# Performance work log

Measured on AMD Instinct MI355X. Metric: run time of the kernel, lower is better.

## Reference

```python
import math
import jax
import jax.numpy as jnp
import numpy as np
from jax import lax

N_FEATURES = 51
WINDOW = 100
EMBED = 12
HIDDEN = math.ceil(0.6 * WINDOW)  # 60
N_PRUNE = math.ceil(0.6 * N_FEATURES * N_FEATURES)  # 1561
BATCH = 8192


def setup_inputs() -> dict:
    key = jax.random.key(0)
    ks = jax.random.split(key, 8)
    x = jax.random.normal(ks[0], (BATCH * N_FEATURES, WINDOW), dtype=jnp.float32)
    embed = jax.random.normal(ks[1], (N_FEATURES, EMBED), dtype=jnp.float32)
    fin = WINDOW + EMBED
    gcn_w = jax.random.normal(ks[2], (WINDOW, fin), dtype=jnp.float32) * (1.0 / np.sqrt(fin))
    gcn_b = jnp.zeros((WINDOW,), dtype=jnp.float32)
    w1 = jax.random.normal(ks[3], (HIDDEN, WINDOW), dtype=jnp.float32) * (1.0 / np.sqrt(WINDOW))
    b1 = jnp.zeros((HIDDEN,), dtype=jnp.float32)
    w2 = jax.random.normal(ks[4], (WINDOW, HIDDEN), dtype=jnp.float32) * (1.0 / np.sqrt(HIDDEN))
    b2 = jnp.zeros((WINDOW,), dtype=jnp.float32)
    return {"x": x, "batch_size": BATCH, "embed": embed, "gcn_w": gcn_w,
            "gcn_b": gcn_b, "w1": w1, "b1": b1, "w2": w2, "b2": b2}


def _prune(A, n):
    """Faithful translation of the serial greedy prune loop."""
    N = A.shape[0]

    def cond(st):
        _, i = st
        return i < n

    def body(st):
        A, i = st
        idx = jnp.argmin(A)
        r, c = idx // N, idx % N
        v = A[r, c]
        ok = ((jnp.sum(A[r]) - v) > 0) | ((jnp.sum(A[:, c]) - v) > 0)
        newval = jnp.where(ok, jnp.float32(0.0), jnp.max(A))
        return (A.at[r, c].set(newval), i + jnp.where(ok, 1, 0))

    A, _ = lax.while_loop(cond, body, (A, jnp.int32(0)))
    return A


def _forward(x, batch_size, embed, gcn_w, gcn_b, w1, b1, w2, b2):
    # --- graph construction from detached embeddings ---
    weights = lax.stop_gradient(embed)                      # [N, E]
    nrm = jnp.linalg.norm(weights, axis=-1)                 # [N]
    cos = (weights @ weights.T) / (nrm[:, None] * nrm[None, :])
    A = _prune(cos, N_PRUNE)
    A = (A != 0).astype(x.dtype)                            # binary adjacency [N, N]
    # GCNConv symmetric normalization with added self-loops
    A_hat = A + jnp.eye(N_FEATURES, dtype=x.dtype)
    dinv = 1.0 / jnp.sqrt(jnp.sum(A_hat, axis=1))
    norm_adj = dinv[:, None] * A_hat * dinv[None, :]        # [N, N]

    # --- features: concat window with node embeddings ---
    all_emb = jnp.tile(embed, (batch_size, 1))              # [B*N, E]
    h = jnp.concatenate([x, all_emb], axis=1)               # [B*N, W+E]
    h = h.reshape(batch_size, N_FEATURES, WINDOW + EMBED)   # [B, N, F]

    # GCNConv: linear transform then normalized aggregation (dropout in eval mode)
    h = h @ gcn_w.T                                         # [B, N, W]
    h = jnp.einsum('ij,bjw->biw', norm_adj, h) + gcn_b      # [B, N, W]
    h = jax.nn.relu(h).reshape(batch_size * N_FEATURES, WINDOW)

    # MLP: Linear -> tanh -> Linear -> tanh
    h = jnp.tanh(h @ w1.T + b1)
    h = jnp.tanh(h @ w2.T + b2)
    return h


def reference(x, batch_size, embed, gcn_w, gcn_b, w1, b1, w2, b2):
    return _forward(x, batch_size, embed, gcn_w, gcn_b, w1, b1, w2, b2)
```

## Files before the change

kernel.cpp:

```cpp
#include <hip/hip_runtime.h>
#include <hip/hip_bf16.h>
#include <stdint.h>

#define NF 51
#define NF2 (51*51)
#define WIN 100
#define EMB 12
#define FIN 112
#define HID 60
#define NPRUNE 1561
#define SORTN 4096

#define WS_WX    0
#define WS_W1    30464
#define WS_ADJ   47872
#define WS_W2    57088
#define WS_D     73216
#define WS_STAGE 47872
#define WS_TOTAL 96064

#define LDS_WX   0
#define LDS_W1   30464
#define LDS_R1X  47872
#define LDS_R1H  79152
#define LDS_R2   110432
#define LDS_TOTAL 142688

typedef _Float16 f16;
typedef _Float16 f16x8 __attribute__((ext_vector_type(8)));
typedef _Float16 f16x4 __attribute__((ext_vector_type(4)));
typedef float f32x4 __attribute__((ext_vector_type(4)));

__device__ __forceinline__ float fast_tanh(float x) {
  float xa = fminf(fmaxf(x, -15.f), 15.f);
  float e = __expf(2.f * xa);
  return (e - 1.f) * __builtin_amdgcn_rcpf(e + 1.f);
}

#define BAR() do { asm volatile("s_waitcnt lgkmcnt(0)" ::: "memory"); \
  __builtin_amdgcn_s_barrier(); asm volatile("" ::: "memory"); } while (0)

__global__ __launch_bounds__(512) void prune_kernel(const float* __restrict__ embed,
                                                    const float* __restrict__ gcn_w,
                                                    const float* __restrict__ gcn_b,
                                                    const float* __restrict__ w1,
                                                    const float* __restrict__ w2,
                                                    void* __restrict__ ws) {
  const int t = threadIdx.x;
  char* wsb = (char*)ws;

  if (blockIdx.x == 1) {
    f16* wxT = (f16*)(wsb + WS_WX);
    for (int u = t; u < 112*136; u += 512) {
      int nn = u / 136, k = u - nn*136;
      wxT[u] = (f16)((nn < WIN && k < WIN) ? gcn_w[nn*FIN + k] : 0.f);
    }
    f16* w1T = (f16*)(wsb + WS_W1);
    for (int u = t; u < 64*136; u += 512) {
      int nn = u / 136, k = u - nn*136;
      w1T[u] = (f16)((nn < HID && k < WIN) ? w1[nn*WIN + k] : 0.f);
    }
    f16* w2T = (f16*)(wsb + WS_W2);
    for (int u = t; u < 112*72; u += 512) {
      int nn = u / 72, k = u - nn*72;
      w2T[u] = (f16)((nn < WIN && k < HID) ? w2[nn*HID + k] : 0.f);
    }
    return;
  }

  __shared__ float sA[NF * 52];
  __shared__ unsigned long long sKey[SORTN];
  __shared__ float sNrm[NF];
  __shared__ float sDinv[NF];
  __shared__ float sRow[NF];
  __shared__ float sCol[NF];
  __shared__ float sRowS[NF];
  __shared__ float sColS[NF];
  __shared__ float sEmb[NF * EMB];
  __shared__ float sE2[NF * EMB];
  __shared__ unsigned char sMask[NF2];
  __shared__ unsigned long long sSusp[64];
  __shared__ int sCand[256];
  __shared__ int sCnt[17];
  __shared__ int sNS;
  __shared__ int sNC;
  __shared__ int sTotal;

  for (int u = t; u < NF * EMB; u += 512) sEmb[u] = embed[u];
  for (int u = t; u < NF2; u += 512) sMask[u] = 0;
  if (t == 0) { sNS = 0; sNC = 0; sTotal = 0; }
  __syncthreads();
  if (t < NF) {
    float s = 0.f;
    for (int e = 0; e < EMB; e++) { float w = sEmb[t*EMB + e]; s += w * w; }
    sNrm[t] = sqrtf(s);
  }
  __syncthreads();
  for (int u = t; u < NF2; u += 512) {
    int r = u / NF, c = u % NF;
    float d = 0.f;
    for (int e = 0; e < EMB; e++) d += sEmb[r*EMB + e] * sEmb[c*EMB + e];
    sA[r*52 + c] = d / (sNrm[r] * sNrm[c]);
  }
  __syncthreads();

  if (t < NF) {
    float rs = 0.f, cs = 0.f;
    for (int j = 0; j < NF; j++) { rs += sA[t*52 + j]; cs += sA[j*52 + t]; }
    sRow[t] = rs; sCol[t] = cs;
  }
  __syncthreads();

  {
    int myCnt = 0;
    for (int u = t; u < NF2; u += 512) {
      int r = u / NF, c = u % NF;
      float v = sA[r*52 + c];
      if (v < 0.f) {
        myCnt++;
        if (sRow[r] <= v && sCol[c] <= v) {
          int slot = atomicAdd(&sNC, 1);
          if (slot < 256) sCand[slot] = u;
        }
      }
    }
    if (myCnt) atomicAdd(&sTotal, myCnt);
  }
  __syncthreads();
  if (sNC <= 256) {
    const int nC = sNC;
    for (int i = t; i < nC; i += 512) {
      int u = sCand[i];
      int r = u / NF, c = u - r*NF;
      float v = sA[r*52 + c];
      float Pr = 0.f, Pc = 0.f;
      for (int j = 0; j < NF; j++) {
        float a = sA[r*52 + j];
        if (a < 0.f && (a < v || (a == v && r*NF + j < u))) Pr -= a;
        float b = sA[j*52 + c];
        if (b < 0.f && (b < v || (b == v && j*NF + c < u))) Pc -= b;
      }
      bool okS = ((sRow[r] + Pr - v) > 0.f) || ((sCol[c] + Pc - v) > 0.f);
      if (!okS) {
        int slot = atomicAdd(&sNS, 1);
        if (slot < 64) {
          unsigned int b = __float_as_uint(v);
          sSusp[slot] = ((unsigned long long)(~b) << 32) | (unsigned int)u;
          sMask[u] = 1;
        }
      }
    }
  }
  __syncthreads();
  const bool fastPath = (sTotal > 0) && (sTotal <= NPRUNE) && (sNC <= 256) && (sNS <= 64);

  if (fastPath) {
    if (t < 64) {
      const int lane = t;
      float mx = -3.0e38f;
      for (int u = lane; u < NF2; u += 64) mx = fmaxf(mx, sA[(u / NF)*52 + (u % NF)]);
      for (int o = 32; o > 0; o >>= 1) mx = fmaxf(mx, __shfl_xor(mx, o, 64));
      if (lane < NF) { sRowS[lane] = 0.f; sColS[lane] = 0.f; }
      const int nS = sNS;
      unsigned long long key = (lane < nS) ? sSusp[lane] : ~0ull;
      for (int k = 2; k <= 64; k <<= 1) {
        for (int j = k >> 1; j > 0; j >>= 1) {
          unsigned long long other = __shfl_xor(key, j, 64);
          bool up = ((lane & k) == 0);
          bool takeMin = (((lane & j) == 0) == up);
          unsigned long long mn = key < other ? key : other;
          unsigned long long mxk = key < other ? other : key;
          key = takeMin ? mn : mxk;
        }
      }
      for (int kk = 0; kk < nS; kk++) {
        unsigned long long kv = __shfl(key, kk, 64);
        unsigned int mb = (unsigned int)(kv >> 32);
        unsigned int idx = (unsigned int)kv;
        float v = __uint_as_float(~mb);
        int r = (int)(idx / NF), c = (int)(idx % NF);
        float pr = 0.f, pc = 0.f;
        if (lane < NF) {
          float a = sA[r*52 + lane];
          if (a < 0.f && !sMask[r*NF + lane] &&
              (a < v || (a == v && (unsigned)(r*NF + lane) < idx))) pr = -a;
          float b = sA[lane*52 + c];
          if (b < 0.f && !sMask[lane*NF + c] &&
              (b < v || (b == v && (unsigned)(lane*NF + c) < idx))) pc = -b;
        }
        for (int o = 32; o > 0; o >>= 1) {
          pr += __shfl_xor(pr, o, 64);
          pc += __shfl_xor(pc, o, 64);
        }
        float sumR = sRow[r] + pr + sRowS[r];
        float sumC = sCol[c] + pc + sColS[c];
        bool ok = ((sumR - v) > 0.f) || ((sumC - v) > 0.f);
        if (lane == 0) {
          if (ok) { sA[r*52 + c] = 0.f; sRowS[r] += -v;     sColS[c] += -v; }
          else    { sA[r*52 + c] = mx;  sRowS[r] += mx - v; sColS[c] += mx - v; }
        }
      }
    }
    __syncthreads();
    for (int u = t; u < NF2; u += 512) {
      int r = u / NF, c = u % NF;
      if (sA[r*52 + c] < 0.f) sA[r*52 + c] = 0.f;
    }
  } else {
    int myCnt = 0;
    for (int u = t; u < NF2; u += 512)
      myCnt += (sA[(u / NF)*52 + (u % NF)] < 0.f) ? 1 : 0;
    int incl = myCnt;
    for (int o = 1; o < 64; o <<= 1) {
      int nb = __shfl_up(incl, o, 64);
      if ((t & 63) >= o) incl += nb;
    }
    if ((t & 63) == 63) sCnt[t >> 6] = incl;
    __syncthreads();
    if (t == 0) {
      int run = 0;
      for (int j = 0; j < 8; j++) { int v = sCnt[j]; sCnt[8 + j] = run; run += v; }
      sCnt[16] = run;
    }
    __syncthreads();
    const int total = sCnt[16];
    const int n = (total <= 2048) ? 2048 : SORTN;
    {
      int cpos = sCnt[8 + (t >> 6)] + (incl - myCnt);
      for (int u = t; u < NF2; u += 512) {
        float v = sA[(u / NF)*52 + (u % NF)];
        if (v < 0.f) {
          unsigned int b = __float_as_uint(v);
          sKey[cpos++] = ((unsigned long long)(~b) << 32) | (unsigned int)u;
        }
      }
      for (int u = total + t; u < n; u += 512) sKey[u] = ~0ull;
    }
    __syncthreads();
    for (int kk = 2; kk <= n; kk <<= 1) {
      for (int jj = kk >> 1; jj > 0; jj >>= 1) {
        for (int u = t; u < n; u += 512) {
          int l = u ^ jj;
          if (l > u) {
            unsigned long long a = sKey[u], b = sKey[l];
            bool up = ((u & kk) == 0);
            if ((a > b) == up) { sKey[u] = b; sKey[l] = a; }
          }
        }
        __syncthreads();
      }
    }

    if (t < 64) {
      const int lane = t;
      float mx = -3.0e38f;
      for (int u = lane; u < NF2; u += 64) mx = fmaxf(mx, sA[(u / NF)*52 + (u % NF)]);
      for (int o = 32; o > 0; o >>= 1) mx = fmaxf(mx, __shfl_xor(mx, o, 64));

      int pruned = 0, pos = 0;
      bool toP2 = false;
      while (pruned < NPRUNE && !toP2) {
        int myi = pos + lane;
        unsigned long long kv = (myi < n) ? sKey[myi] : ~0ull;
        unsigned int mb  = (unsigned int)(kv >> 32);
        unsigned int idx = (unsigned int)kv;
        unsigned int vb  = (mb & 0x80000000u) ? (mb & 0x7FFFFFFFu) : ~mb;
        float v = __uint_as_float(vb);
        bool elig = (v < 0.f) && (idx < (unsigned)NF2);
        int r = 0, c2 = 0; bool okl = false;
        if (elig) {
          r = (int)(idx / NF); c2 = (int)(idx % NF);
          float sr = sRow[r], sc = sCol[c2];
          okl = ((sr - v) > 0.f) || ((sc - v) > 0.f);
        }
        unsigned long long bal = __ballot(okl);
        unsigned long long nb = ~bal;
        int nok = (nb == 0ull) ? 64 : (int)__builtin_ctzll(nb);
        int rem = NPRUNE - pruned;
        int take = nok < rem ? nok : rem;
        if (lane < take) {
          sA[r*52 + c2] = 0.f;
          atomicAdd(&sRow[r], -v);
          atomicAdd(&sCol[c2], -v);
        }
        pruned += take; pos += take;
        if (pruned >= NPRUNE) break;
        if (take == 64) continue;
        unsigned int bvb = (unsigned int)__builtin_amdgcn_readlane((int)vb, take);
        int bidx = __builtin_amdgcn_readlane((int)idx, take);
        float bv = __uint_as_float(bvb);
        if (!(bv < 0.f) || bidx >= NF2) { toP2 = true; break; }
        int br = bidx / NF, bc = bidx % NF;
        float sr = sRow[br], sc = sCol[bc];
        bool ok = ((sr - bv) > 0.f) || ((sc - bv) > 0.f);
        if (ok) {
          if (lane == 0) {
            sA[br*52 + bc] = 0.f;
            sRow[br] = sr - bv; sCol[bc] = sc - bv;
          }
          pruned++; pos++;
        } else {
          if (lane == 0) {
            sA[br*52 + bc] = mx;
            sRow[br] = sr + (mx - bv); sCol[bc] = sc + (mx - bv);
          }
          pos++;
        }
      }
      if (toP2) {
        for (int guard = 0; guard < 40000 && pruned < NPRUNE; guard++) {
          float bv = 3.0e38f; int bidx = NF2;
          for (int u = lane; u < NF2; u += 64) {
            float v = sA[(u / NF)*52 + (u % NF)];
            if (v < bv) { bv = v; bidx = u; }
          }
          for (int o = 32; o > 0; o >>= 1) {
            float ov = __shfl_xor(bv, o, 64);
            int  oi = __shfl_xor(bidx, o, 64);
            if (ov < bv || (ov == bv && oi < bidx)) { bv = ov; bidx = oi; }
          }
          int br = bidx / NF, bc = bidx % NF;
          float sr = sRow[br], sc = sCol[bc];
          bool ok = ((sr - bv) > 0.f) || ((sc - bv) > 0.f);
          if (ok) {
            if (bv == 0.f) break;
            if (lane == 0) { sA[br*52+bc] = 0.f; sRow[br] = sr - bv; sCol[bc] = sc - bv; }
            pruned++;
          } else {
            if (bv == mx) break;
            if (lane == 0) { sA[br*52+bc] = mx; sRow[br] = sr + (mx-bv); sCol[bc] = sc + (mx-bv); }
          }
        }
      }
    }
  }
  __syncthreads();

  if (t < NF) {
    float deg = 0.f;
    for (int j = 0; j < NF; j++) {
      float a = sA[t*52 + j];
      float bin = (a != 0.f) ? 1.f : 0.f;
      if (j == t) bin += 1.f;
      deg += bin;
    }
    sDinv[t] = 1.f / sqrtf(deg);
  }
  __syncthreads();

  float* sN = (float*)sKey;
  for (int u = t; u < NF * 52; u += 512) {
    int r = u / 52, c = u % 52;
    float v = 0.f;
    if (c < NF) {
      float a = sA[r*52 + c];
      float bin = (a != 0.f) ? 1.f : 0.f;
      if (r == c) bin += 1.f;
      v = sDinv[r] * bin * sDinv[c];
    }
    sN[u] = v;
  }
  __syncthreads();

  for (int u = t; u < NF * EMB; u += 512) {
    int i = u / EMB, e = u % EMB;
    float s2 = 0.f;
    for (int j = 0; j < NF; j++) s2 += sN[i*52 + j] * sEmb[j*EMB + e];
    sE2[u] = s2;
  }

  f16* adjT = (f16*)(wsb + WS_ADJ);
  for (int u = t; u < 64*72; u += 512) {
    int r = u / 72, k = u % 72;
    adjT[u] = (f16)((r < NF && k < NF) ? sN[r*52 + k] : 0.f);
  }
  __syncthreads();
  float* Dp = (float*)(wsb + WS_D);
  for (int u = t; u < NF * 112; u += 512) {
    int i = u / 112, w = u % 112;
    float s2 = 0.f;
    if (w < WIN) {
      for (int e = 0; e < EMB; e++) s2 += sE2[i*EMB + e] * gcn_w[w*FIN + WIN + e];
      s2 += gcn_b[w];
    }
    Dp[u] = s2;
  }
}

__global__ __launch_bounds__(512, 1) void forward_kernel(
    const float* __restrict__ x, const float* __restrict__ b1g,
    const float* __restrict__ b2g, const void* __restrict__ ws,
    float* __restrict__ out, int nPairs, int ppb) {
  __shared__ __align__(16) char smem[LDS_TOTAL];
  f16* wxT = (f16*)(smem + LDS_WX);
  f16* w1T = (f16*)(smem + LDS_W1);
  f16* sX  = (f16*)(smem + LDS_R1X);
  f16* sH  = (f16*)(smem + LDS_R1H);
  f16* yT  = (f16*)(smem + LDS_R2);
  f16* h3  = (f16*)(smem + LDS_R2);

  const int t = threadIdx.x;
  const int wv = t >> 6, lane = t & 63;
  const int c = lane & 15, g = lane >> 4;
  const int s = wv >> 2, mt = wv & 3;
  const int rowA = 51*s + 16*mt + c;

  {
    const f32x4* w4 = (const f32x4*)ws;
    f32x4* s4 = (f32x4*)smem;
    #pragma unroll
    for (int u = 0; u < 6; u++) { int i = t + u*512; if (i < 2992) s4[i] = w4[i]; }
    f32x4 z = {0.f,0.f,0.f,0.f};
    f32x4* za = (f32x4*)(smem + LDS_R1X);
    #pragma unroll
    for (int u = 0; u < 12; u++) { int i = t + u*512; if (i < 5926) za[i] = z; }
  }

  const int pair0 = blockIdx.x * ppb;
  float4 p0, p1, p2, p3, p4;
  if (pair0 < nPairs) {
    const float4* xb = (const float4*)(x + (size_t)pair0 * 10200);
    p0 = xb[t]; p1 = xb[t+512]; p2 = xb[t+1024]; p3 = xb[t+1536];
    if (t < 502) p4 = xb[t+2048];
  }

  const char* wsb = (const char*)ws;
  const f16* adjG = (const f16*)(wsb + WS_ADJ);
  const f16* w2G  = (const f16*)(wsb + WS_W2);
  const float* DG = (const float*)(wsb + WS_D);

  f16x8 adjf[4][2];
  #pragma unroll
  for (int N = 0; N < 4; N++) {
    const f16* bp = &adjG[(16*N + c)*72 + 8*g];
    adjf[N][0] = *(const f16x8*)(bp + 0);
    adjf[N][1] = *(const f16x8*)(bp + 32);
  }
  f16x8 w2f[7][2];
  #pragma unroll
  for (int N = 0; N < 7; N++) {
    const f16* ap = &w2G[(16*N + c)*72 + 8*g];
    w2f[N][0] = *(const f16x8*)(ap + 0);
    w2f[N][1] = *(const f16x8*)(ap + 32);
  }
  const int s2a = (wv == 7) ? 1 : 0;
  const int wta = (wv == 7) ? 0 : wv;
  const int wtb = wv + 1;
  float4 dA[4], dB[4];
  {
    const float4 zf = {0.f,0.f,0.f,0.f};
    #pragma unroll
    for (int N = 0; N < 4; N++) {
      int nd = 16*N + c;
      dA[N] = (nd < NF) ? *(const float4*)&DG[nd*112 + 16*wta + 4*g] : zf;
      dB[N] = (wv < 6 && nd < NF) ? *(const float4*)&DG[nd*112 + 16*wtb + 4*g] : zf;
    }
  }
  float4 b1f[4], b2f[7];
  {
    const float4 zf = {0.f,0.f,0.f,0.f};
    #pragma unroll
    for (int N = 0; N < 4; N++) {
      int colb = 16*N + 4*g;
      b1f[N] = (colb < HID) ? *(const float4*)&b1g[colb] : zf;
    }
    #pragma unroll
    for (int N = 0; N < 7; N++) {
      int colb = 16*N + 4*g;
      b2f[N] = (colb < WIN) ? *(const float4*)&b2g[colb] : zf;
    }
  }
  __syncthreads();

  if (pair0 < nPairs) {
    #define STV(PV, V) { int row = (V)/25, q4 = ((V)%25)*4; \
      f16x4 hv = {(f16)(PV).x,(f16)(PV).y,(f16)(PV).z,(f16)(PV).w}; \
      *(f16x4*)&sX[row*136 + q4] = hv; }
    STV(p0, t); STV(p1, t+512); STV(p2, t+1024); STV(p3, t+1536);
    if (t < 502) STV(p4, t+2048);
  }

  #pragma unroll 1
  for (int p = 0; p < ppb; p++) {
    const int pairIdx = pair0 + p;
    const bool valid = pairIdx < nPairs;

    BAR();

    if (p + 1 < ppb && pairIdx + 1 < nPairs) {
      const float4* xb = (const float4*)(x + (size_t)(pairIdx+1) * 10200);
      p0 = xb[t]; p1 = xb[t+512]; p2 = xb[t+1024]; p3 = xb[t+1536];
      if (t < 502) p4 = xb[t+2048];
    }

    if (valid) {
      const f16* aB = &sX[rowA*136];
      const f16x8 a0 = *(const f16x8*)(aB +  0 + 8*g);
      const f16x8 a1 = *(const f16x8*)(aB + 32 + 8*g);
      const f16x8 a2 = *(const f16x8*)(aB + 64 + 8*g);
      const f16x8 a3 = *(const f16x8*)(aB + 96 + 8*g);
      f16* yTs = yT + s*8064;
      const int nodeW = 16*mt + 4*g;
      #pragma unroll
      for (int N = 0; N < 7; N++) {
        const f16* bp = &wxT[(16*N + c)*136 + 8*g];
        f32x4 acc = {0.f,0.f,0.f,0.f};
        acc = __builtin_amdgcn_mfma_f32_16x16x32_f16(a0, *(const f16x8*)(bp +  0), acc, 0, 0, 0);
        acc = __builtin_amdgcn_mfma_f32_16x16x32_f16(a1, *(const f16x8*)(bp + 32), acc, 0, 0, 0);
        acc = __builtin_amdgcn_mfma_f32_16x16x32_f16(a2, *(const f16x8*)(bp + 64), acc, 0, 0, 0);
        acc = __builtin_amdgcn_mfma_f32_16x16x32_f16(a3, *(const f16x8*)(bp + 96), acc, 0, 0, 0);
        const int col = 16*N + c;
        if (mt < 3) {
          f16x4 hv = {(f16)acc[0],(f16)acc[1],(f16)acc[2],(f16)acc[3]};
          *(f16x4*)&yTs[col*72 + nodeW] = hv;
        } else {
          #pragma unroll
          for (int r2 = 0; r2 < 4; r2++)
            if (nodeW + r2 < NF) yTs[col*72 + nodeW + r2] = (f16)acc[r2];
        }
      }
    }
    BAR();

    if (valid) {
      {
        const f16* ap = &yT[s2a*8064 + (16*wta + c)*72 + 8*g];
        const f16x8 a0 = *(const f16x8*)(ap + 0);
        const f16x8 a1 = *(const f16x8*)(ap + 32);
        #pragma unroll
        for (int N = 0; N < 4; N++) {
          f32x4 acc = {0.f,0.f,0.f,0.f};
          acc = __builtin_amdgcn_mfma_f32_16x16x32_f16(a0, adjf[N][0], acc, 0, 0, 0);
          acc = __builtin_amdgcn_mfma_f32_16x16x32_f16(a1, adjf[N][1], acc, 0, 0, 0);
          const int nd = 16*N + c;
          if (nd < NF) {
            const float4 dv = dA[N];
            f16x4 hv = {(f16)fmaxf(acc[0]+dv.x,0.f),(f16)fmaxf(acc[1]+dv.y,0.f),
                        (f16)fmaxf(acc[2]+dv.z,0.f),(f16)fmaxf(acc[3]+dv.w,0.f)};
            *(f16x4*)&sH[(51*s2a + nd)*136 + 16*wta + 4*g] = hv;
          }
        }
      }
      if (wv < 6) {
        const f16* ap = &yT[8064 + (16*wtb + c)*72 + 8*g];
        const f16x8 a0 = *(const f16x8*)(ap + 0);
        const f16x8 a1 = *(const f16x8*)(ap + 32);
        #pragma unroll
        for (int N = 0; N < 4; N++) {
          f32x4 acc = {0.f,0.f,0.f,0.f};
          acc = __builtin_amdgcn_mfma_f32_16x16x32_f16(a0, adjf[N][0], acc, 0, 0, 0);
          acc = __builtin_amdgcn_mfma_f32_16x16x32_f16(a1, adjf[N][1], acc, 0, 0, 0);
          const int nd = 16*N + c;
          if (nd < NF) {
            const float4 dv = dB[N];
            f16x4 hv = {(f16)fmaxf(acc[0]+dv.x,0.f),(f16)fmaxf(acc[1]+dv.y,0.f),
                        (f16)fmaxf(acc[2]+dv.z,0.f),(f16)fmaxf(acc[3]+dv.w,0.f)};
            *(f16x4*)&sH[(51 + nd)*136 + 16*wtb + 4*g] = hv;
          }
        }
      }
    }
    BAR();

    if (valid) {
      const f16* bB = &sH[rowA*136 + 8*g];
      const f16x8 hb0 = *(const f16x8*)(bB +  0);
      const f16x8 hb1 = *(const f16x8*)(bB + 32);
      const f16x8 hb2 = *(const f16x8*)(bB + 64);
      const f16x8 hb3 = *(const f16x8*)(bB + 96);
      #pragma unroll
      for (int N = 0; N < 4; N++) {
        const f16* ap = &w1T[(16*N + c)*136 + 8*g];
        f32x4 acc = {0.f,0.f,0.f,0.f};
        acc = __builtin_amdgcn_mfma_f32_16x16x32_f16(*(const f16x8*)(ap +  0), hb0, acc, 0, 0, 0);
        acc = __builtin_amdgcn_mfma_f32_16x16x32_f16(*(const f16x8*)(ap + 32), hb1, acc, 0, 0, 0);
        acc = __builtin_amdgcn_mfma_f32_16x16x32_f16(*(const f16x8*)(ap + 64), hb2, acc, 0, 0, 0);
        acc = __builtin_amdgcn_mfma_f32_16x16x32_f16(*(const f16x8*)(ap + 96), hb3, acc, 0, 0, 0);
        const int colb = 16*N + 4*g;
        const float4 bv = b1f[N];
        f16x4 hv = {(f16)fast_tanh(acc[0]+bv.x),(f16)fast_tanh(acc[1]+bv.y),
                    (f16)fast_tanh(acc[2]+bv.z),(f16)fast_tanh(acc[3]+bv.w)};
        *(f16x4*)&h3[rowA*72 + colb] = hv;
      }
    }
    asm volatile("s_waitcnt lgkmcnt(0)" ::: "memory");
    __builtin_amdgcn_sched_barrier(0);

    if (valid) {
      const f16* bB = &h3[rowA*72 + 8*g];
      const f16x8 hb0 = *(const f16x8*)(bB +  0);
      const f16x8 hb1 = *(const f16x8*)(bB + 32);
      const bool rowOk = (16*mt + c) < NF;
      float* ob = out + (size_t)pairIdx * 10200 + (size_t)rowA * 100;
      #pragma unroll
      for (int N = 0; N < 7; N++) {
        f32x4 acc = {0.f,0.f,0.f,0.f};
        acc = __builtin_amdgcn_mfma_f32_16x16x32_f16(w2f[N][0], hb0, acc, 0, 0, 0);
        acc = __builtin_amdgcn_mfma_f32_16x16x32_f16(w2f[N][1], hb1, acc, 0, 0, 0);
        const int colb = 16*N + 4*g;
        if (rowOk && colb < WIN) {
          const float4 bv = b2f[N];
          float4 ov = {fast_tanh(acc[0]+bv.x), fast_tanh(acc[1]+bv.y),
                       fast_tanh(acc[2]+bv.z), fast_tanh(acc[3]+bv.w)};
          *(float4*)&ob[colb] = ov;
        }
      }
    }

    if (p + 1 < ppb && pairIdx + 1 < nPairs) {
      #define STV2(PV, V) { int row = (V)/25, q4 = ((V)%25)*4; \
        f16x4 hv = {(f16)(PV).x,(f16)(PV).y,(f16)(PV).z,(f16)(PV).w}; \
        *(f16x4*)&sX[row*136 + q4] = hv; }
      STV2(p0, t); STV2(p1, t+512); STV2(p2, t+1024); STV2(p3, t+1536);
      if (t < 502) STV2(p4, t+2048);
      #undef STV2
    }
  }
}

extern "C" void kernel_launch(void* const* d_in, const int* in_sizes, int n_in,
                              void* d_out, int out_size, void* d_ws, size_t ws_size,
                              hipStream_t stream) {
  const float* x     = (const float*)d_in[0];
  const float* embed = (const float*)d_in[2];
  const float* gcn_w = (const float*)d_in[3];
  const float* gcn_b = (const float*)d_in[4];
  const float* w1    = (const float*)d_in[5];
  const float* b1    = (const float*)d_in[6];
  const float* w2    = (const float*)d_in[7];
  const float* b2    = (const float*)d_in[8];
  float* out = (float*)d_out;

  const int batch = in_sizes[0] / (NF * WIN);
  const int nPairs = batch / 2;
  const int blocks = 256;
  const int ppb = (nPairs + blocks - 1) / blocks;

  prune_kernel<<<2, 512, 0, stream>>>(embed, gcn_w, gcn_b, w1, w2, d_ws);
  forward_kernel<<<blocks, 512, 0, stream>>>(x, b1, b2, d_ws, out, nPairs, ppb);
}
```

Before: 133.0 us.

## Split block into two 4-wave groups running staggered three-phase sample pipeline

The block now works as two independent 4-wave groups, each with its own LDS region and 16 samples. The three stages (GCN linear, adjacency aggregation, MLP plus store) run as phases, and the second group is offset by one phase. The intent is that different stages from the two groups overlap between barriers, so MFMA, LDS and global-store work interleave instead of all waves doing the same stage at once. In exchange, each sample needs three barrier-separated steps, LDS use grows slightly, and work per barrier interval is uneven between the groups.

```diff
diff --git a/kernel.cpp b/kernel.cpp
--- a/kernel.cpp
+++ b/kernel.cpp
@@ -10,6 +10,7 @@
 #define HID 60
 #define NPRUNE 1561
 #define SORTN 4096
+#define NPG 16
 
 #define WS_WX    0
 #define WS_W1    30464
@@ -21,10 +22,9 @@
 
 #define LDS_WX   0
 #define LDS_W1   30464
-#define LDS_R1X  47872
-#define LDS_R1H  79152
-#define LDS_R2   110432
-#define LDS_TOTAL 142688
+#define LDS_GRP  47872
+#define GRP_SPAN 50944
+#define LDS_TOTAL 149760
 
 typedef _Float16 f16;
 typedef _Float16 f16x8 __attribute__((ext_vector_type(8)));
@@ -390,20 +390,22 @@
 __global__ __launch_bounds__(512, 1) void forward_kernel(
     const float* __restrict__ x, const float* __restrict__ b1g,
     const float* __restrict__ b2g, const void* __restrict__ ws,
-    float* __restrict__ out, int nPairs, int ppb) {
+    float* __restrict__ out, int nSamp) {
   __shared__ __align__(16) char smem[LDS_TOTAL];
   f16* wxT = (f16*)(smem + LDS_WX);
   f16* w1T = (f16*)(smem + LDS_W1);
-  f16* sX  = (f16*)(smem + LDS_R1X);
-  f16* sH  = (f16*)(smem + LDS_R1H);
-  f16* yT  = (f16*)(smem + LDS_R2);
-  f16* h3  = (f16*)(smem + LDS_R2);
 
   const int t = threadIdx.x;
   const int wv = t >> 6, lane = t & 63;
+  const int gq = wv >> 2, wq = wv & 3;
+  const int tl = t & 255;
   const int c = lane & 15, g = lane >> 4;
-  const int s = wv >> 2, mt = wv & 3;
-  const int rowA = 51*s + 16*mt + c;
+  const int rowA1 = 16*wq + c;
+  char* grp = smem + LDS_GRP + gq * GRP_SPAN;
+  f16* sXg = (f16*)(grp);
+  f16* sHg = (f16*)(grp + 17408);
+  f16* yTg = (f16*)(grp + 34816);
+  f16* h3g = yTg;
 
   {
     const f32x4* w4 = (const f32x4*)ws;
@@ -411,17 +413,9 @@
     #pragma unroll
     for (int u = 0; u < 6; u++) { int i = t + u*512; if (i < 2992) s4[i] = w4[i]; }
     f32x4 z = {0.f,0.f,0.f,0.f};
-    f32x4* za = (f32x4*)(smem + LDS_R1X);
+    f32x4* za = (f32x4*)(smem + LDS_GRP);
     #pragma unroll
-    for (int u = 0; u < 12; u++) { int i = t + u*512; if (i < 5926) za[i] = z; }
-  }
-
-  const int pair0 = blockIdx.x * ppb;
-  float4 p0, p1, p2, p3, p4;
-  if (pair0 < nPairs) {
-    const float4* xb = (const float4*)(x + (size_t)pair0 * 10200);
-    p0 = xb[t]; p1 = xb[t+512]; p2 = xb[t+1024]; p3 = xb[t+1536];
-    if (t < 502) p4 = xb[t+2048];
+    for (int u = 0; u < 13; u++) { int i = t + u*512; if (i < 6368) za[i] = z; }
   }
 
   const char* wsb = (const char*)ws;
@@ -443,17 +437,14 @@
     w2f[N][0] = *(const f16x8*)(ap + 0);
     w2f[N][1] = *(const f16x8*)(ap + 32);
   }
-  const int s2a = (wv == 7) ? 1 : 0;
-  const int wta = (wv == 7) ? 0 : wv;
-  const int wtb = wv + 1;
   float4 dA[4], dB[4];
   {
     const float4 zf = {0.f,0.f,0.f,0.f};
     #pragma unroll
     for (int N = 0; N < 4; N++) {
       int nd = 16*N + c;
-      dA[N] = (nd < NF) ? *(const float4*)&DG[nd*112 + 16*wta + 4*g] : zf;
-      dB[N] = (wv < 6 && nd < NF) ? *(const float4*)&DG[nd*112 + 16*wtb + 4*g] : zf;
+      dA[N] = (nd < NF) ? *(const float4*)&DG[nd*112 + 16*wq + 4*g] : zf;
+      dB[N] = (wq < 3 && nd < NF) ? *(const float4*)&DG[nd*112 + 16*(wq+4) + 4*g] : zf;
     }
   }
   float4 b1f[4], b2f[7];
@@ -472,150 +463,151 @@
   }
   __syncthreads();
 
-  if (pair0 < nPairs) {
-    #define STV(PV, V) { int row = (V)/25, q4 = ((V)%25)*4; \
-      f16x4 hv = {(f16)(PV).x,(f16)(PV).y,(f16)(PV).z,(f16)(PV).w}; \
-      *(f16x4*)&sX[row*136 + q4] = hv; }
-    STV(p0, t); STV(p1, t+512); STV(p2, t+1024); STV(p3, t+1536);
-    if (t < 502) STV(p4, t+2048);
-  }
+  const int sBase = blockIdx.x * (2*NPG) + gq * NPG;
+  float4 p0, p1, p2, p3, p4;
+  #define LOADP(SI) { const float4* xb = (const float4*)(x + (size_t)(SI) * 5100); \
+    p0 = xb[tl]; p1 = xb[tl+256]; p2 = xb[tl+512]; p3 = xb[tl+768]; \
+    if (tl < 251) p4 = xb[tl+1024]; }
+  #define STV1(PV, V) { int row = (V)/25, q4 = ((V)%25)*4; \
+    f16x4 hv = {(f16)(PV).x,(f16)(PV).y,(f16)(PV).z,(f16)(PV).w}; \
+    *(f16x4*)&sXg[row*136 + q4] = hv; }
+  #define STVX() { STV1(p0, tl) STV1(p1, tl+256) STV1(p2, tl+512) STV1(p3, tl+768) \
+                   if (tl < 251) STV1(p4, tl+1024) }
+
+  if (sBase < nSamp) LOADP(sBase);
+  if (gq == 0) {
+    if (sBase < nSamp) STVX();
+    if (sBase + 1 < nSamp) LOADP(sBase + 1);
+  }
+  BAR();
+
+  const int phS1 = gq ? 1 : 0;
+  const int phS2 = gq ? 2 : 1;
 
   #pragma unroll 1
-  for (int p = 0; p < ppb; p++) {
-    const int pairIdx = pair0 + p;
-    const bool valid = pairIdx < nPairs;
-
-    BAR();
-
-    if (p + 1 < ppb && pairIdx + 1 < nPairs) {
-      const float4* xb = (const float4*)(x + (size_t)(pairIdx+1) * 10200);
-      p0 = xb[t]; p1 = xb[t+512]; p2 = xb[t+1024]; p3 = xb[t+1536];
-      if (t < 502) p4 = xb[t+2048];
-    }
-
-    if (valid) {
-      const f16* aB = &sX[rowA*136];
-      const f16x8 a0 = *(const f16x8*)(aB +  0 + 8*g);
-      const f16x8 a1 = *(const f16x8*)(aB + 32 + 8*g);
-      const f16x8 a2 = *(const f16x8*)(aB + 64 + 8*g);
-      const f16x8 a3 = *(const f16x8*)(aB + 96 + 8*g);
-      f16* yTs = yT + s*8064;
-      const int nodeW = 16*mt + 4*g;
-      #pragma unroll
-      for (int N = 0; N < 7; N++) {
-        const f16* bp = &wxT[(16*N + c)*136 + 8*g];
-        f32x4 acc = {0.f,0.f,0.f,0.f};
-        acc = __builtin_amdgcn_mfma_f32_16x16x32_f16(a0, *(const f16x8*)(bp +  0), acc, 0, 0, 0);
-        acc = __builtin_amdgcn_mfma_f32_16x16x32_f16(a1, *(const f16x8*)(bp + 32), acc, 0, 0, 0);
-        acc = __builtin_amdgcn_mfma_f32_16x16x32_f16(a2, *(const f16x8*)(bp + 64), acc, 0, 0, 0);
-        acc = __builtin_amdgcn_mfma_f32_16x16x32_f16(a3, *(const f16x8*)(bp + 96), acc, 0, 0, 0);
-        const int col = 16*N + c;
-        if (mt < 3) {
-          f16x4 hv = {(f16)acc[0],(f16)acc[1],(f16)acc[2],(f16)acc[3]};
-          *(f16x4*)&yTs[col*72 + nodeW] = hv;
-        } else {
+  for (int k = 0; k < 3*NPG + 1; k++) {
+    const int ph = k % 3;
+    const int kd3 = k / 3;
+    const f32x4 zacc = {0.f,0.f,0.f,0.f};
+
+    if (ph == phS1) {
+      if (kd3 < NPG && sBase + kd3 < nSamp) {
+        const f16* aB = &sXg[rowA1*136];
+        const f16x8 a0 = *(const f16x8*)(aB +  0 + 8*g);
+        const f16x8 a1 = *(const f16x8*)(aB + 32 + 8*g);
+        const f16x8 a2 = *(const f16x8*)(aB + 64 + 8*g);
+        const f16x8 a3 = *(const f16x8*)(aB + 96 + 8*g);
+        const int nodeW = 16*wq + 4*g;
+        #pragma unroll
+        for (int N = 0; N < 7; N++) {
+          const f16* bp = &wxT[(16*N + c)*136 + 8*g];
+          f32x4 acc = zacc;
+          acc = __builtin_amdgcn_mfma_f32_16x16x32_f16(a0, *(const f16x8*)(bp +  0), acc, 0, 0, 0);
+          acc = __builtin_amdgcn_mfma_f32_16x16x32_f16(a1, *(const f16x8*)(bp + 32), acc, 0, 0, 0);
+          acc = __builtin_amdgcn_mfma_f32_16x16x32_f16(a2, *(const f16x8*)(bp + 64), acc, 0, 0, 0);
+          acc = __builtin_amdgcn_mfma_f32_16x16x32_f16(a3, *(const f16x8*)(bp + 96), acc, 0, 0, 0);
+          const int col = 16*N + c;
+          if (wq < 3) {
+            f16x4 hv = {(f16)acc[0],(f16)acc[1],(f16)acc[2],(f16)acc[3]};
+            *(f16x4*)&yTg[col*72 + nodeW] = hv;
+          } else {
+            #pragma unroll
+            for (int r2 = 0; r2 < 4; r2++)
+              if (nodeW + r2 < NF) yTg[col*72 + nodeW + r2] = (f16)acc[r2];
+          }
+        }
+      }
+    } else if (ph == phS2) {
+      if (kd3 < NPG && sBase + kd3 < nSamp) {
+        {
+          const f16* ap = &yTg[(16*wq + c)*72 + 8*g];
+          const f16x8 a0 = *(const f16x8*)(ap + 0);
+          const f16x8 a1 = *(const f16x8*)(ap + 32);
           #pragma unroll
-          for (int r2 = 0; r2 < 4; r2++)
-            if (nodeW + r2 < NF) yTs[col*72 + nodeW + r2] = (f16)acc[r2];
-        }
-      }
-    }
-    BAR();
-
-    if (valid) {
-      {
-        const f16* ap = &yT[s2a*8064 + (16*wta + c)*72 + 8*g];
-        const f16x8 a0 = *(const f16x8*)(ap + 0);
-        const f16x8 a1 = *(const f16x8*)(ap + 32);
+          for (int N = 0; N < 4; N++) {
+            f32x4 acc = zacc;
+            acc = __builtin_amdgcn_mfma_f32_16x16x32_f16(a0, adjf[N][0], acc, 0, 0, 0);
+            acc = __builtin_amdgcn_mfma_f32_16x16x32_f16(a1, adjf[N][1], acc, 0, 0, 0);
+            const int nd = 16*N + c;
+            if (nd < NF) {
+              const float4 dv = dA[N];
+              f16x4 hv = {(f16)fmaxf(acc[0]+dv.x,0.f),(f16)fmaxf(acc[1]+dv.y,0.f),
+                          (f16)fmaxf(acc[2]+dv.z,0.f),(f16)fmaxf(acc[3]+dv.w,0.f)};
+              *(f16x4*)&sHg[nd*136 + 16*wq + 4*g] = hv;
+            }
+          }
+        }
+        if (wq < 3) {
+          const f16* ap = &yTg[(16*(wq+4) + c)*72 + 8*g];
+          const f16x8 a0 = *(const f16x8*)(ap + 0);
+          const f16x8 a1 = *(const f16x8*)(ap + 32);
+          #pragma unroll
+          for (int N = 0; N < 4; N++) {
+            f32x4 acc = zacc;
+            acc = __builtin_amdgcn_mfma_f32_16x16x32_f16(a0, adjf[N][0], acc, 0, 0, 0);
+            acc = __builtin_amdgcn_mfma_f32_16x16x32_f16(a1, adjf[N][1], acc, 0, 0, 0);
+            const int nd = 16*N + c;
+            if (nd < NF) {
+              const float4 dv = dB[N];
+              f16x4 hv = {(f16)fmaxf(acc[0]+dv.x,0.f),(f16)fmaxf(acc[1]+dv.y,0.f),
+                          (f16)fmaxf(acc[2]+dv.z,0.f),(f16)fmaxf(acc[3]+dv.w,0.f)};
+              *(f16x4*)&sHg[nd*136 + 16*(wq+4) + 4*g] = hv;
+            }
+          }
+        }
+      }
+    } else {
+      const int m = kd3 - gq;
+      if (m >= 0 && m < NPG && sBase + m < nSamp) {
+        const int sIdx = sBase + m;
+        const f16* bB = &sHg[rowA1*136 + 8*g];
+        const f16x8 hb0 = *(const f16x8*)(bB +  0);
+        const f16x8 hb1 = *(const f16x8*)(bB + 32);
+        const f16x8 hb2 = *(const f16x8*)(bB + 64);
+        const f16x8 hb3 = *(const f16x8*)(bB + 96);
         #pragma unroll
         for (int N = 0; N < 4; N++) {
-          f32x4 acc = {0.f,0.f,0.f,0.f};
-          acc = __builtin_amdgcn_mfma_f32_16x16x32_f16(a0, adjf[N][0], acc, 0, 0, 0);
-          acc = __builtin_amdgcn_mfma_f32_16x16x32_f16(a1, adjf[N][1], acc, 0, 0, 0);
-          const int nd = 16*N + c;
-          if (nd < NF) {
-            const float4 dv = dA[N];
-            f16x4 hv = {(f16)fmaxf(acc[0]+dv.x,0.f),(f16)fmaxf(acc[1]+dv.y,0.f),
-                        (f16)fmaxf(acc[2]+dv.z,0.f),(f16)fmaxf(acc[3]+dv.w,0.f)};
-            *(f16x4*)&sH[(51*s2a + nd)*136 + 16*wta + 4*g] = hv;
-          }
-        }
-      }
-      if (wv < 6) {
-        const f16* ap = &yT[8064 + (16*wtb + c)*72 + 8*g];
-        const f16x8 a0 = *(const f16x8*)(ap + 0);
-        const f16x8 a1 = *(const f16x8*)(ap + 32);
+          const f16* ap = &w1T[(16*N + c)*136 + 8*g];
+          f32x4 acc = zacc;
+          acc = __builtin_amdgcn_mfma_f32_16x16x32_f16(*(const f16x8*)(ap +  0), hb0, acc, 0, 0, 0);
+          acc = __builtin_amdgcn_mfma_f32_16x16x32_f16(*(const f16x8*)(ap + 32), hb1, acc, 0, 0, 0);
+          acc = __builtin_amdgcn_mfma_f32_16x16x32_f16(*(const f16x8*)(ap + 64), hb2, acc, 0, 0, 0);
+          acc = __builtin_amdgcn_mfma_f32_16x16x32_f16(*(const f16x8*)(ap + 96), hb3, acc, 0, 0, 0);
+          const int colb = 16*N + 4*g;
+          const float4 bv = b1f[N];
+          f16x4 hv = {(f16)fast_tanh(acc[0]+bv.x),(f16)fast_tanh(acc[1]+bv.y),
+                      (f16)fast_tanh(acc[2]+bv.z),(f16)fast_tanh(acc[3]+bv.w)};
+          *(f16x4*)&h3g[rowA1*72 + colb] = hv;
+        }
+        asm volatile("s_waitcnt lgkmcnt(0)" ::: "memory");
+        __builtin_amdgcn_sched_barrier(0);
+        const f16* bC = &h3g[rowA1*72 + 8*g];
+        const f16x8 hc0 = *(const f16x8*)(bC +  0);
+        const f16x8 hc1 = *(const f16x8*)(bC + 32);
+        const bool rowOk = rowA1 < NF;
+        float* ob = out + (size_t)sIdx * 5100 + (size_t)rowA1 * 100;
         #pragma unroll
-        for (int N = 0; N < 4; N++) {
-          f32x4 acc = {0.f,0.f,0.f,0.f};
-          acc = __builtin_amdgcn_mfma_f32_16x16x32_f16(a0, adjf[N][0], acc, 0, 0, 0);
-          acc = __builtin_amdgcn_mfma_f32_16x16x32_f16(a1, adjf[N][1], acc, 0, 0, 0);
-          const int nd = 16*N + c;
-          if (nd < NF) {
-            const float4 dv = dB[N];
-            f16x4 hv = {(f16)fmaxf(acc[0]+dv.x,0.f),(f16)fmaxf(acc[1]+dv.y,0.f),
-                        (f16)fmaxf(acc[2]+dv.z,0.f),(f16)fmaxf(acc[3]+dv.w,0.f)};
-            *(f16x4*)&sH[(51 + nd)*136 + 16*wtb + 4*g] = hv;
-          }
-        }
-      }
+        for (int N = 0; N < 7; N++) {
+          f32x4 acc = zacc;
+          acc = __builtin_amdgcn_mfma_f32_16x16x32_f16(w2f[N][0], hc0, acc, 0, 0, 0);
+          acc = __builtin_amdgcn_mfma_f32_16x16x32_f16(w2f[N][1], hc1, acc, 0, 0, 0);
+          const int colb = 16*N + 4*g;
+          if (rowOk && colb < WIN) {
+            const float4 bv = b2f[N];
+            float4 ov = {fast_tanh(acc[0]+bv.x), fast_tanh(acc[1]+bv.y),
+                         fast_tanh(acc[2]+bv.z), fast_tanh(acc[3]+bv.w)};
+            *(float4*)&ob[colb] = ov;
+          }
+        }
+      }
+      if (m + 1 < NPG && sBase + m + 1 < nSamp) STVX();
+      if (m + 2 < NPG && sBase + m + 2 < nSamp) LOADP(sBase + m + 2);
     }
     BAR();
-
-    if (valid) {
-      const f16* bB = &sH[rowA*136 + 8*g];
-      const f16x8 hb0 = *(const f16x8*)(bB +  0);
-      const f16x8 hb1 = *(const f16x8*)(bB + 32);
-      const f16x8 hb2 = *(const f16x8*)(bB + 64);
-      const f16x8 hb3 = *(const f16x8*)(bB + 96);
-      #pragma unroll
-      for (int N = 0; N < 4; N++) {
-        const f16* ap = &w1T[(16*N + c)*136 + 8*g];
-        f32x4 acc = {0.f,0.f,0.f,0.f};
-        acc = __builtin_amdgcn_mfma_f32_16x16x32_f16(*(const f16x8*)(ap +  0), hb0, acc, 0, 0, 0);
-        acc = __builtin_amdgcn_mfma_f32_16x16x32_f16(*(const f16x8*)(ap + 32), hb1, acc, 0, 0, 0);
-        acc = __builtin_amdgcn_mfma_f32_16x16x32_f16(*(const f16x8*)(ap + 64), hb2, acc, 0, 0, 0);
-        acc = __builtin_amdgcn_mfma_f32_16x16x32_f16(*(const f16x8*)(ap + 96), hb3, acc, 0, 0, 0);
-        const int colb = 16*N + 4*g;
-        const float4 bv = b1f[N];
-        f16x4 hv = {(f16)fast_tanh(acc[0]+bv.x),(f16)fast_tanh(acc[1]+bv.y),
-                    (f16)fast_tanh(acc[2]+bv.z),(f16)fast_tanh(acc[3]+bv.w)};
-        *(f16x4*)&h3[rowA*72 + colb] = hv;
-      }
-    }
-    asm volatile("s_waitcnt lgkmcnt(0)" ::: "memory");
-    __builtin_amdgcn_sched_barrier(0);
-
-    if (valid) {
-      const f16* bB = &h3[rowA*72 + 8*g];
-      const f16x8 hb0 = *(const f16x8*)(bB +  0);
-      const f16x8 hb1 = *(const f16x8*)(bB + 32);
-      const bool rowOk = (16*mt + c) < NF;
-      float* ob = out + (size_t)pairIdx * 10200 + (size_t)rowA * 100;
-      #pragma unroll
-      for (int N = 0; N < 7; N++) {
-        f32x4 acc = {0.f,0.f,0.f,0.f};
-        acc = __builtin_amdgcn_mfma_f32_16x16x32_f16(w2f[N][0], hb0, acc, 0, 0, 0);
-        acc = __builtin_amdgcn_mfma_f32_16x16x32_f16(w2f[N][1], hb1, acc, 0, 0, 0);
-        const int colb = 16*N + 4*g;
-        if (rowOk && colb < WIN) {
-          const float4 bv = b2f[N];
-          float4 ov = {fast_tanh(acc[0]+bv.x), fast_tanh(acc[1]+bv.y),
-                       fast_tanh(acc[2]+bv.z), fast_tanh(acc[3]+bv.w)};
-          *(float4*)&ob[colb] = ov;
-        }
-      }
-    }
-
-    if (p + 1 < ppb && pairIdx + 1 < nPairs) {
-      #define STV2(PV, V) { int row = (V)/25, q4 = ((V)%25)*4; \
-        f16x4 hv = {(f16)(PV).x,(f16)(PV).y,(f16)(PV).z,(f16)(PV).w}; \
-        *(f16x4*)&sX[row*136 + q4] = hv; }
-      STV2(p0, t); STV2(p1, t+512); STV2(p2, t+1024); STV2(p3, t+1536);
-      if (t < 502) STV2(p4, t+2048);
-      #undef STV2
-    }
-  }
+  }
+  #undef LOADP
+  #undef STV1
+  #undef STVX
 }
 
 extern "C" void kernel_launch(void* const* d_in, const int* in_sizes, int n_in,
@@ -632,10 +624,8 @@
   float* out = (float*)d_out;
 
   const int batch = in_sizes[0] / (NF * WIN);
-  const int nPairs = batch / 2;
   const int blocks = 256;
-  const int ppb = (nPairs + blocks - 1) / blocks;
 
   prune_kernel<<<2, 512, 0, stream>>>(embed, gcn_w, gcn_b, w1, w2, d_ws);
-  forward_kernel<<<blocks, 512, 0, stream>>>(x, b1, b2, d_ws, out, nPairs, ppb);
+  forward_kernel<<<blocks, 512, 0, stream>>>(x, b1, b2, d_ws, out, batch);
 }
```

Result: slower. 145.9 us (+9.6%).
